# Kernel tuning notes

Measured on AMD Instinct MI355X. Metric: run time of the kernel, lower is better.

## Reference

```python
import jax, jax.numpy as jnp
import numpy as np

T, B, D = 512, 64, 1536
MAX_RADIUS = 0.999
INIT_RADIUS = 0.99
EPS = 1e-8


def setup_inputs() -> dict:
    key = jax.random.key(0)
    ks = jax.random.split(key, 5)
    # xavier_uniform bound for square [D, D] weight
    bound = float(np.sqrt(6.0 / (D + D)))
    p = INIT_RADIUS / MAX_RADIUS
    init_logit = float(np.log(p / (1.0 - p)))
    u = jax.random.normal(ks[4], (D,), dtype=jnp.float32)
    u = u / jnp.linalg.norm(u)
    return {
        "x": jax.random.normal(ks[0], (T, B, D), dtype=jnp.float32),
        "z": jax.random.normal(ks[1], (T, B, D), dtype=jnp.float32),
        "h0": jnp.zeros((B, D), dtype=jnp.float32),
        "W_x": jax.random.uniform(ks[2], (D, D), jnp.float32, -bound, bound),
        "W_h": jax.random.uniform(ks[3], (D, D), jnp.float32, -bound, bound),
        "b": jnp.zeros((D,), dtype=jnp.float32),
        "log_radius": jnp.full((1,), init_logit, dtype=jnp.float32),
        "u": u,
    }


def _spectral_norm_W_h(W_h, log_radius, u):
    """W_h scaled so its (power-iteration estimated) spectral radius = target."""
    target = jax.nn.sigmoid(log_radius)[0] * MAX_RADIUS
    # 3 power-iteration steps, done under stop_gradient (torch uses no_grad)
    v = u
    for _ in range(3):
        v = W_h.T @ u
        v = v / (jnp.linalg.norm(v) + EPS)
        u = W_h @ v
        u = u / (jnp.linalg.norm(u) + EPS)
    u = jax.lax.stop_gradient(u)
    v = jax.lax.stop_gradient(v)
    sigma = jnp.abs(u @ W_h @ v)
    return W_h * (target / (sigma + EPS))


def reference(x, z, h0, W_x, W_h, b, log_radius, u):
    Wh = _spectral_norm_W_h(W_h, log_radius, u)

    def step(h_prev, xz):
        x_t, z_t = xz  # [B, D] each
        h_new = jnp.tanh(x_t @ W_x.T + h_prev @ Wh.T + b)
        out_t = h_new * jax.nn.silu(z_t)
        return h_new, (h_new, out_t)

    _, (hs, outs) = jax.lax.scan(step, h0, (x, z))  # hs, outs: [T, B, D]
    h_all = jnp.concatenate([h0[None], hs], axis=0)  # [T+1, B, D]
    return outs, h_all
```

## Files before the change

### kernel.cpp

```cpp
#include <hip/hip_runtime.h>

#define DD 1536
#define TT 512
#define BB 64
#define BD (BB*DD)
#define TBD (TT*BD)
#define NWG 96

typedef __attribute__((ext_vector_type(8))) short short8;
typedef __attribute__((ext_vector_type(4))) float f32x4;

__device__ __forceinline__ short f2bf(float f) {
  unsigned u = __builtin_bit_cast(unsigned, f);
  u += 0x7FFFu + ((u >> 16) & 1u);
  return (short)(u >> 16);
}

__device__ __forceinline__ void st_coh_b32(int* p, int v) {
  asm volatile("global_store_dword %0, %1, off sc0 sc1" :: "v"(p), "v"(v) : "memory");
}

#define LDQ(dst, addr, imm) \
  asm volatile("global_load_dwordx4 %0, %1, off offset:" #imm " sc0 sc1" \
               : "=v"(dst) : "v"(addr) : "memory")


__global__ __launch_bounds__(256) void k_matvec_row(
    const float* __restrict__ W, const float* __restrict__ x, float* __restrict__ y) {
  int wave = (blockIdx.x * 256 + threadIdx.x) >> 6;
  int lane = threadIdx.x & 63;
  const float* Wr = W + (size_t)wave * DD;
  float acc = 0.f;
  for (int j = lane; j < DD; j += 64) acc += Wr[j] * x[j];
  for (int off = 32; off; off >>= 1) acc += __shfl_down(acc, off, 64);
  if (lane == 0) y[wave] = acc;
}

__global__ __launch_bounds__(256) void k_matvec_colf(
    const float* __restrict__ W, const float* __restrict__ x, float* __restrict__ y) {
  int j = blockIdx.x * 256 + threadIdx.x;
  float a0 = 0.f, a1 = 0.f, a2 = 0.f, a3 = 0.f;
  for (int i = 0; i < DD; i += 4) {
    a0 += W[(size_t)(i + 0) * DD + j] * x[i + 0];
    a1 += W[(size_t)(i + 1) * DD + j] * x[i + 1];
    a2 += W[(size_t)(i + 2) * DD + j] * x[i + 2];
    a3 += W[(size_t)(i + 3) * DD + j] * x[i + 3];
  }
  y[j] = (a0 + a1) + (a2 + a3);
}

__global__ __launch_bounds__(256) void k_scale(
    const float* __restrict__ t5, const float* __restrict__ t6,
    const float* __restrict__ log_radius, float* __restrict__ s_out) {
  __shared__ float red[8];
  int tid = threadIdx.x;
  float a5 = 0.f, a6 = 0.f;
  for (int i = tid; i < DD; i += 256) { float v5 = t5[i], v6 = t6[i]; a5 += v5*v5; a6 += v6*v6; }
  for (int off = 32; off; off >>= 1) { a5 += __shfl_down(a5, off, 64); a6 += __shfl_down(a6, off, 64); }
  int w = tid >> 6, lane = tid & 63;
  if (lane == 0) { red[w] = a5; red[4 + w] = a6; }
  __syncthreads();
  if (tid == 0) {
    float s5 = red[0] + red[1] + red[2] + red[3];
    float s6 = red[4] + red[5] + red[6] + red[7];
    float sigma = sqrtf(s6 / s5);
    float lr = log_radius[0];
    float target = 0.999f / (1.f + expf(-lr));
    s_out[0] = target / (sigma + 1e-8f);
  }
}

__global__ __launch_bounds__(256) void k_conv(
    const float* __restrict__ in, short* __restrict__ out, int n8) {
  int i = blockIdx.x * 256 + threadIdx.x;
  int stride = gridDim.x * 256;
  for (; i < n8; i += stride) {
    const float4* p = (const float4*)(in + (size_t)i * 8);
    float4 a = p[0], b = p[1];
    short8 v;
    v[0]=f2bf(a.x); v[1]=f2bf(a.y); v[2]=f2bf(a.z); v[3]=f2bf(a.w);
    v[4]=f2bf(b.x); v[5]=f2bf(b.y); v[6]=f2bf(b.z); v[7]=f2bf(b.w);
    *(short8*)(out + (size_t)i * 8) = v;
  }
}

__global__ __launch_bounds__(256) void k_gemm_xA(
    const float* __restrict__ x, const float* __restrict__ Wx,
    const float* __restrict__ bias, float* __restrict__ Aout) {
  __shared__ short As[128 * 64];
  __shared__ short Bs[128 * 64];
  const int tid = threadIdx.x;
  const int lane = tid & 63;
  const int w = tid >> 6;
  const int n0 = blockIdx.x * 128;
  const int m0 = blockIdx.y * 128;
  const int mq = (w >> 1) * 64;
  const int nq = (w & 1) * 64;

  f32x4 acc[4][4];
#pragma unroll
  for (int i = 0; i < 4; ++i)
#pragma unroll
    for (int j = 0; j < 4; ++j) acc[i][j] = (f32x4){0.f, 0.f, 0.f, 0.f};

  const int r0 = tid >> 3;
  const int c8 = tid & 7;

  for (int k0 = 0; k0 < DD; k0 += 64) {
    __syncthreads();
#pragma unroll
    for (int c = 0; c < 4; ++c) {
      int row = c * 32 + r0;
      const float4* gx = (const float4*)(x + (size_t)(m0 + row) * DD + k0 + c8 * 8);
      const float4* gw = (const float4*)(Wx + (size_t)(n0 + row) * DD + k0 + c8 * 8);
      float4 x0 = gx[0], x1 = gx[1];
      float4 w0 = gw[0], w1 = gw[1];
      short8 xv, wv;
      xv[0]=f2bf(x0.x); xv[1]=f2bf(x0.y); xv[2]=f2bf(x0.z); xv[3]=f2bf(x0.w);
      xv[4]=f2bf(x1.x); xv[5]=f2bf(x1.y); xv[6]=f2bf(x1.z); xv[7]=f2bf(x1.w);
      wv[0]=f2bf(w0.x); wv[1]=f2bf(w0.y); wv[2]=f2bf(w0.z); wv[3]=f2bf(w0.w);
      wv[4]=f2bf(w1.x); wv[5]=f2bf(w1.y); wv[6]=f2bf(w1.z); wv[7]=f2bf(w1.w);
      int so = (row * 64 + c8 * 8) ^ ((row & 7) << 3);
      *(short8*)&As[so] = xv;
      *(short8*)&Bs[so] = wv;
    }
    __syncthreads();
#pragma unroll
    for (int kk = 0; kk < 64; kk += 32) {
      short8 af[4], bfr[4];
#pragma unroll
      for (int f = 0; f < 4; ++f) {
        int ar = mq + f * 16 + (lane & 15);
        int k = kk + ((lane >> 4) << 3);
        af[f] = *(const short8*)&As[(ar * 64 + k) ^ ((ar & 7) << 3)];
        int br = nq + f * 16 + (lane & 15);
        bfr[f] = *(const short8*)&Bs[(br * 64 + k) ^ ((br & 7) << 3)];
      }
#pragma unroll
      for (int i = 0; i < 4; ++i)
#pragma unroll
        for (int j = 0; j < 4; ++j)
          acc[i][j] = __builtin_amdgcn_mfma_f32_16x16x32_bf16(af[i], bfr[j], acc[i][j], 0, 0, 0);
    }
  }
#pragma unroll
  for (int i = 0; i < 4; ++i) {
    int rbase = m0 + mq + i * 16 + ((lane >> 4) << 2);
#pragma unroll
    for (int j = 0; j < 4; ++j) {
      int col = n0 + nq + j * 16 + (lane & 15);
      float bv = bias[col];
#pragma unroll
      for (int r = 0; r < 4; ++r)
        Aout[(size_t)(rbase + r) * DD + col] = acc[i][j][r] + bv;
    }
  }
}

__global__ __launch_bounds__(256) void k_gemm_b(
    const short* __restrict__ xb, const short* __restrict__ Wxb,
    const float* __restrict__ bias, float* __restrict__ Aout) {
  __shared__ short As[128 * 64];
  __shared__ short Bs[128 * 64];
  const int tid = threadIdx.x;
  const int lane = tid & 63;
  const int w = tid >> 6;
  const int n0 = blockIdx.x * 128;
  const int m0 = blockIdx.y * 128;
  const int mq = (w >> 1) * 64;
  const int nq = (w & 1) * 64;

  f32x4 acc[4][4];
#pragma unroll
  for (int i = 0; i < 4; ++i)
#pragma unroll
    for (int j = 0; j < 4; ++j) acc[i][j] = (f32x4){0.f, 0.f, 0.f, 0.f};

  const int r0 = tid >> 3;
  const int c8 = tid & 7;

  for (int k0 = 0; k0 < DD; k0 += 64) {
    __syncthreads();
#pragma unroll
    for (int c = 0; c < 4; ++c) {
      int row = c * 32 + r0;
      short8 xv = *(const short8*)(xb  + (size_t)(m0 + row) * DD + k0 + c8 * 8);
      short8 wv = *(const short8*)(Wxb + (size_t)(n0 + row) * DD + k0 + c8 * 8);
      int so = (row * 64 + c8 * 8) ^ ((row & 7) << 3);
      *(short8*)&As[so] = xv;
      *(short8*)&Bs[so] = wv;
    }
    __syncthreads();
#pragma unroll
    for (int kk = 0; kk < 64; kk += 32) {
      short8 af[4], bfr[4];
#pragma unroll
      for (int f = 0; f < 4; ++f) {
        int ar = mq + f * 16 + (lane & 15);
        int k = kk + ((lane >> 4) << 3);
        af[f] = *(const short8*)&As[(ar * 64 + k) ^ ((ar & 7) << 3)];
        int br = nq + f * 16 + (lane & 15);
        bfr[f] = *(const short8*)&Bs[(br * 64 + k) ^ ((br & 7) << 3)];
      }
#pragma unroll
      for (int i = 0; i < 4; ++i)
#pragma unroll
        for (int j = 0; j < 4; ++j)
          acc[i][j] = __builtin_amdgcn_mfma_f32_16x16x32_bf16(af[i], bfr[j], acc[i][j], 0, 0, 0);
    }
  }
#pragma unroll
  for (int i = 0; i < 4; ++i) {
    int rbase = m0 + mq + i * 16 + ((lane >> 4) << 2);
#pragma unroll
    for (int j = 0; j < 4; ++j) {
      int col = n0 + nq + j * 16 + (lane & 15);
      float bv = bias[col];
#pragma unroll
      for (int r = 0; r < 4; ++r)
        Aout[(size_t)(rbase + r) * DD + col] = acc[i][j][r] + bv;
    }
  }
}

__global__ __launch_bounds__(512, 1) void k_recur(
    const float* __restrict__ Wh, const float* __restrict__ h0,
    const float* __restrict__ z, const float* __restrict__ sp,
    float* __restrict__ outs, float* __restrict__ hall,
    short* __restrict__ hbuf, int* __restrict__ flags) {
  __shared__ f32x4 REDS[2][2048];
  const int tid = threadIdx.x;
  const int lane = tid & 63;
  const int wv = tid >> 6;
  const int wgid = blockIdx.x;
  const int fg = wgid >> 2;
  const int mq = wgid & 3;
  const int n0 = fg * 64;
  const int m0 = mq * 16;

  const int nl = lane & 15;
  const int hi8 = (lane >> 4) << 3;
  const int kw = wv * 192;

  short8 bfr[6][4];
#pragma unroll
  for (int j = 0; j < 6; ++j)
#pragma unroll
    for (int f = 0; f < 4; ++f) {
      const float* gp = Wh + (size_t)(n0 + f * 16 + nl) * DD + kw + j * 32 + hi8;
      float4 a0 = *(const float4*)gp;
      float4 a1 = *(const float4*)(gp + 4);
      short8 v;
      v[0]=f2bf(a0.x); v[1]=f2bf(a0.y); v[2]=f2bf(a0.z); v[3]=f2bf(a0.w);
      v[4]=f2bf(a1.x); v[5]=f2bf(a1.y); v[6]=f2bf(a1.z); v[7]=f2bf(a1.w);
      bfr[j][f] = v;
    }

  const int r = wv + ((lane >> 5) << 3);
  const int c = (lane & 31) * 2;
  const int f0 = c >> 4;
  const int c15 = c & 15;
  const int l2a = ((r >> 2) << 4) | c15;
  const int l2b = l2a + 1;
  const int ri = r & 3;
  const size_t eidx = (size_t)(m0 + r) * DD + n0 + c;
  const size_t aoff = (size_t)(m0 + nl) * DD + kw + hi8;

  int* myflag = flags + ((mq * 24 + fg) * 8 + wv) * 16;
  const int* cflag = flags + (((mq * 24 + wv * 3 + (lane >> 3)) * 8) + (lane & 7)) * 16;

  short* pg = hbuf;
  short* pn = hbuf + BD;
  short* pq = hbuf + 2 * BD;

  {
    float vx = h0[eidx], vy = h0[eidx + 1];
    hall[eidx] = vx; hall[eidx + 1] = vy;
    unsigned pk = (unsigned)(unsigned short)f2bf(vx)
                | ((unsigned)(unsigned short)f2bf(vy) << 16);
    st_coh_b32((int*)(pg + eidx), (int)pk);
  }
  const float sv = sp[0];
  asm volatile("s_waitcnt vmcnt(0)" ::: "memory");
  if (lane == 0) st_coh_b32(myflag, 1);

  float pa = outs[eidx], pay = outs[eidx + 1];
  float pz = z[eidx], pzy = z[eidx + 1];

  for (int t = 0; t < TT; ++t) {
    const bool last = (t == TT - 1);

    if (lane < 24) {
      int it = 0;
      for (;;) {
        int v = __hip_atomic_load(cflag, __ATOMIC_RELAXED, __HIP_MEMORY_SCOPE_AGENT);
        if (v >= t + 1 || ++it > (1 << 20)) break;
        __builtin_amdgcn_s_sleep(1);
      }
    }

    const short* hp = pg + aoff;
    short8 a0, a1, a2, a3, a4, a5;
    LDQ(a0, hp, 0);
    LDQ(a1, hp, 64);
    LDQ(a2, hp, 128);
    LDQ(a3, hp, 192);
    LDQ(a4, hp, 256);
    LDQ(a5, hp, 320);
    asm volatile("s_waitcnt vmcnt(0)" ::: "memory");
    __builtin_amdgcn_sched_barrier(0);

    f32x4 acc0 = (f32x4){0,0,0,0}, acc1 = (f32x4){0,0,0,0};
    f32x4 acc2 = (f32x4){0,0,0,0}, acc3 = (f32x4){0,0,0,0};
#define MF4(aa, j) \
    acc0 = __builtin_amdgcn_mfma_f32_16x16x32_bf16(aa, bfr[j][0], acc0, 0, 0, 0); \
    acc1 = __builtin_amdgcn_mfma_f32_16x16x32_bf16(aa, bfr[j][1], acc1, 0, 0, 0); \
    acc2 = __builtin_amdgcn_mfma_f32_16x16x32_bf16(aa, bfr[j][2], acc2, 0, 0, 0); \
    acc3 = __builtin_amdgcn_mfma_f32_16x16x32_bf16(aa, bfr[j][3], acc3, 0, 0, 0);
    MF4(a0, 0) MF4(a1, 1) MF4(a2, 2) MF4(a3, 3) MF4(a4, 4) MF4(a5, 5)
#undef MF4

    f32x4* R = REDS[t & 1];
    {
      const int lsw = lane ^ ((lane >> 5) & 1);
#define WR(f, accv) { f32x4 wv_; \
      wv_[(0 + f) & 3] = accv[0]; wv_[(1 + f) & 3] = accv[1]; \
      wv_[(2 + f) & 3] = accv[2]; wv_[(3 + f) & 3] = accv[3]; \
      R[wv * 256 + f * 64 + lsw] = wv_; }
      WR(0, acc0) WR(1, acc1) WR(2, acc2) WR(3, acc3)
#undef WR
    }
    __syncthreads();
    const float* Rf = (const float*)R;
    const int ia = (f0 * 64 + (l2a ^ ((l2a >> 5) & 1))) * 4 + ((ri + f0) & 3);
    const int ib = (f0 * 64 + (l2b ^ ((l2b >> 5) & 1))) * 4 + ((ri + f0) & 3);
    float s0 = 0.f, s1 = 0.f;
#pragma unroll
    for (int w2 = 0; w2 < 8; ++w2) {
      s0 += Rf[w2 * 1024 + ia];
      s1 += Rf[w2 * 1024 + ib];
    }

    float h0v = tanhf(pa + sv * s0);
    float h1v = tanhf(pay + sv * s1);
    if (!last) {
      unsigned pk = (unsigned)(unsigned short)f2bf(h0v)
                  | ((unsigned)(unsigned short)f2bf(h1v) << 16);
      st_coh_b32((int*)(pn + eidx), (int)pk);
      asm volatile("s_waitcnt vmcnt(0)" ::: "memory");
      if (lane == 0) st_coh_b32(myflag, t + 2);
    }

    size_t tb = (size_t)t * BD;
    hall[tb + BD + eidx] = h0v;
    hall[tb + BD + eidx + 1] = h1v;
    outs[tb + eidx]     = h0v * (pz  / (1.f + __expf(-pz)));
    outs[tb + eidx + 1] = h1v * (pzy / (1.f + __expf(-pzy)));
    if (!last) {
      size_t nb = tb + BD + eidx;
      pa = outs[nb]; pay = outs[nb + 1];
      pz = z[nb];    pzy = z[nb + 1];
    }
    short* tmp = pg; pg = pn; pn = pq; pq = tmp;
  }
}

extern "C" void kernel_launch(void* const* d_in, const int* in_sizes, int n_in,
                              void* d_out, int out_size, void* d_ws, size_t ws_size,
                              hipStream_t stream) {
  const float* x  = (const float*)d_in[0];
  const float* z  = (const float*)d_in[1];
  const float* h0 = (const float*)d_in[2];
  const float* Wx = (const float*)d_in[3];
  const float* Wh = (const float*)d_in[4];
  const float* b  = (const float*)d_in[5];
  const float* lr = (const float*)d_in[6];
  const float* u  = (const float*)d_in[7];

  float* outs = (float*)d_out;
  float* hall = outs + (size_t)TBD;

  char* ws = (char*)d_ws;
  float* vA = (float*)ws;
  float* vB = vA + DD;
  float* vC = vB + DD;
  float* vD = vC + DD;
  float* sS = vD + DD;
  int*   flags = (int*)(ws + 32768);
  short* hbuf  = (short*)(ws + 131072);

  short* xb  = (short*)(ws + ((size_t)16 << 20));
  short* Wxb = xb + (size_t)TBD;
  const size_t need = ((size_t)16 << 20) + ((size_t)TBD + (size_t)DD * DD) * 2 + 1024;
  const bool big = ws_size >= need;

  if (big) {
    hipLaunchKernelGGL(k_conv, dim3(2048), dim3(256), 0, stream, x,  xb,  TBD / 8);
    hipLaunchKernelGGL(k_conv, dim3(512),  dim3(256), 0, stream, Wx, Wxb, DD * DD / 8);
    hipLaunchKernelGGL(k_gemm_b, dim3(12, 256), dim3(256), 0, stream, xb, Wxb, b, outs);
  } else {
    hipLaunchKernelGGL(k_gemm_xA, dim3(12, 256), dim3(256), 0, stream, x, Wx, b, outs);
  }

  hipLaunchKernelGGL(k_matvec_colf, dim3(6),   dim3(256), 0, stream, Wh, u,  vA);
  hipLaunchKernelGGL(k_matvec_row,  dim3(384), dim3(256), 0, stream, Wh, vA, vB);
  hipLaunchKernelGGL(k_matvec_colf, dim3(6),   dim3(256), 0, stream, Wh, vB, vA);
  hipLaunchKernelGGL(k_matvec_row,  dim3(384), dim3(256), 0, stream, Wh, vA, vB);
  hipLaunchKernelGGL(k_matvec_colf, dim3(6),   dim3(256), 0, stream, Wh, vB, vC);
  hipLaunchKernelGGL(k_matvec_row,  dim3(384), dim3(256), 0, stream, Wh, vC, vD);
  hipLaunchKernelGGL(k_scale, dim3(1), dim3(256), 0, stream, vC, vD, lr, sS);

  hipMemsetAsync(flags, 0, 49152, stream);

  void* args[8] = {(void*)&Wh, (void*)&h0, (void*)&z, (void*)&sS,
                   (void*)&outs, (void*)&hall, (void*)&hbuf, (void*)&flags};
  hipLaunchCooperativeKernel((const void*)k_recur, dim3(NWG), dim3(512), args, 0, stream);
}
```

Before: 2.466 ms.

## Fuse power-iteration matvecs and scale into one cooperative kernel

Replaces the seven small power-iteration launches (column and row matvecs plus the scale kernel) with a single 384-workgroup cooperative kernel that uses flag-based grid barriers between phases. The column matvec is split across 96 workgroups, each handling a slice of rows and combining partial sums with atomics, instead of running on only 6 blocks. The workspace is relaid out and zeroed with one memset, which replaces the separate flag memset. This targets launch overhead and the poor parallelism of the serial column matvec, at the cost of spin-wait barriers and atomic accumulation order.

```diff
diff --git a/kernel.cpp b/kernel.cpp
--- a/kernel.cpp
+++ b/kernel.cpp
@@ -24,49 +24,93 @@
   asm volatile("global_load_dwordx4 %0, %1, off offset:" #imm " sc0 sc1" \
                : "=v"(dst) : "v"(addr) : "memory")
 
-
-__global__ __launch_bounds__(256) void k_matvec_row(
-    const float* __restrict__ W, const float* __restrict__ x, float* __restrict__ y) {
-  int wave = (blockIdx.x * 256 + threadIdx.x) >> 6;
-  int lane = threadIdx.x & 63;
-  const float* Wr = W + (size_t)wave * DD;
-  float acc = 0.f;
-  for (int j = lane; j < DD; j += 64) acc += Wr[j] * x[j];
-  for (int off = 32; off; off >>= 1) acc += __shfl_down(acc, off, 64);
-  if (lane == 0) y[wave] = acc;
-}
-
-__global__ __launch_bounds__(256) void k_matvec_colf(
-    const float* __restrict__ W, const float* __restrict__ x, float* __restrict__ y) {
-  int j = blockIdx.x * 256 + threadIdx.x;
-  float a0 = 0.f, a1 = 0.f, a2 = 0.f, a3 = 0.f;
-  for (int i = 0; i < DD; i += 4) {
-    a0 += W[(size_t)(i + 0) * DD + j] * x[i + 0];
-    a1 += W[(size_t)(i + 1) * DD + j] * x[i + 1];
-    a2 += W[(size_t)(i + 2) * DD + j] * x[i + 2];
-    a3 += W[(size_t)(i + 3) * DD + j] * x[i + 3];
-  }
-  y[j] = (a0 + a1) + (a2 + a3);
-}
-
-__global__ __launch_bounds__(256) void k_scale(
-    const float* __restrict__ t5, const float* __restrict__ t6,
-    const float* __restrict__ log_radius, float* __restrict__ s_out) {
+__device__ __forceinline__ float ld_coh_f(const float* p) {
+  return __hip_atomic_load(p, __ATOMIC_RELAXED, __HIP_MEMORY_SCOPE_AGENT);
+}
+
+__global__ __launch_bounds__(256) void k_power(
+    const float* __restrict__ Wh, const float* __restrict__ u,
+    const float* __restrict__ lr, float* __restrict__ base,
+    int* __restrict__ pflags) {
   __shared__ float red[8];
-  int tid = threadIdx.x;
-  float a5 = 0.f, a6 = 0.f;
-  for (int i = tid; i < DD; i += 256) { float v5 = t5[i], v6 = t6[i]; a5 += v5*v5; a6 += v6*v6; }
-  for (int off = 32; off; off >>= 1) { a5 += __shfl_down(a5, off, 64); a6 += __shfl_down(a6, off, 64); }
-  int w = tid >> 6, lane = tid & 63;
-  if (lane == 0) { red[w] = a5; red[4 + w] = a6; }
-  __syncthreads();
-  if (tid == 0) {
-    float s5 = red[0] + red[1] + red[2] + red[3];
-    float s6 = red[4] + red[5] + red[6] + red[7];
-    float sigma = sqrtf(s6 / s5);
-    float lr = log_radius[0];
-    float target = 0.999f / (1.f + expf(-lr));
-    s_out[0] = target / (sigma + 1e-8f);
+  const int tid = threadIdx.x;
+  const int lane = tid & 63;
+  const int wgid = blockIdx.x;
+
+  float* vA = base;
+  float* vB = base + 1536;
+  float* vC = base + 3072;
+  float* vD = base + 4608;
+  float* vE = base + 6144;
+  float* vF = base + 7680;
+  float* sS = base + 9216;
+
+  auto bar = [&](int gen) {
+    asm volatile("s_waitcnt vmcnt(0)" ::: "memory");
+    __syncthreads();
+    if (tid == 0) st_coh_b32(pflags + wgid * 16, gen);
+    int it = 0;
+    for (;;) {
+      int v0 = __hip_atomic_load(pflags + tid * 16, __ATOMIC_RELAXED, __HIP_MEMORY_SCOPE_AGENT);
+      int v1 = (tid < 128)
+        ? __hip_atomic_load(pflags + (256 + tid) * 16, __ATOMIC_RELAXED, __HIP_MEMORY_SCOPE_AGENT)
+        : gen;
+      if ((v0 >= gen && v1 >= gen) || ++it > (1 << 20)) break;
+      __builtin_amdgcn_s_sleep(1);
+    }
+    __syncthreads();
+  };
+
+  auto colf = [&](const float* src, float* dst) {
+    if (wgid < 96) {
+      int jt = wgid % 6, ic = wgid / 6;
+      int j = jt * 256 + tid;
+      int i0 = ic * 96;
+      float a0 = 0.f, a1 = 0.f, a2 = 0.f, a3 = 0.f;
+      for (int i = i0; i < i0 + 96; i += 4) {
+        a0 += Wh[(size_t)(i + 0) * DD + j] * ld_coh_f(src + i + 0);
+        a1 += Wh[(size_t)(i + 1) * DD + j] * ld_coh_f(src + i + 1);
+        a2 += Wh[(size_t)(i + 2) * DD + j] * ld_coh_f(src + i + 2);
+        a3 += Wh[(size_t)(i + 3) * DD + j] * ld_coh_f(src + i + 3);
+      }
+      atomicAdd(&dst[j], (a0 + a1) + (a2 + a3));
+    }
+  };
+
+  auto rowf = [&](const float* src, float* dst) {
+    int row = wgid * 4 + (tid >> 6);
+    const float* Wr = Wh + (size_t)row * DD;
+    float acc = 0.f;
+    for (int j = lane; j < DD; j += 64) acc += Wr[j] * ld_coh_f(src + j);
+    for (int off = 32; off; off >>= 1) acc += __shfl_down(acc, off, 64);
+    if (lane == 0) st_coh_b32((int*)&dst[row], __builtin_bit_cast(int, acc));
+  };
+
+  colf(u,  vA); bar(1);
+  rowf(vA, vB); bar(2);
+  colf(vB, vC); bar(3);
+  rowf(vC, vD); bar(4);
+  colf(vD, vE); bar(5);
+  rowf(vE, vF); bar(6);
+
+  if (wgid == 0) {
+    float a5 = 0.f, a6 = 0.f;
+    for (int i = tid; i < DD; i += 256) {
+      float v5 = ld_coh_f(vE + i), v6 = ld_coh_f(vF + i);
+      a5 += v5 * v5; a6 += v6 * v6;
+    }
+    for (int off = 32; off; off >>= 1) { a5 += __shfl_down(a5, off, 64); a6 += __shfl_down(a6, off, 64); }
+    int w = tid >> 6;
+    if (lane == 0) { red[w] = a5; red[4 + w] = a6; }
+    __syncthreads();
+    if (tid == 0) {
+      float s5 = red[0] + red[1] + red[2] + red[3];
+      float s6 = red[4] + red[5] + red[6] + red[7];
+      float sigma = sqrtf(s6 / s5);
+      float lrv = lr[0];
+      float target = 0.999f / (1.f + expf(-lrv));
+      sS[0] = target / (sigma + 1e-8f);
+    }
   }
 }
 
@@ -381,18 +425,18 @@
   float* hall = outs + (size_t)TBD;
 
   char* ws = (char*)d_ws;
-  float* vA = (float*)ws;
-  float* vB = vA + DD;
-  float* vC = vB + DD;
-  float* vD = vC + DD;
-  float* sS = vD + DD;
-  int*   flags = (int*)(ws + 32768);
+  float* base  = (float*)ws;
+  float* sS    = base + 9216;
+  int*   flags = (int*)(ws + 40960);
+  int*   pflg  = (int*)(ws + 90112);
   short* hbuf  = (short*)(ws + 131072);
-
-  short* xb  = (short*)(ws + ((size_t)16 << 20));
-  short* Wxb = xb + (size_t)TBD;
-  const size_t need = ((size_t)16 << 20) + ((size_t)TBD + (size_t)DD * DD) * 2 + 1024;
+  short* xb    = (short*)(ws + ((size_t)1 << 20));
+  short* Wxb   = xb + (size_t)TBD;
+
+  const size_t need = ((size_t)1 << 20) + ((size_t)TBD + (size_t)DD * DD) * 2 + 1024;
   const bool big = ws_size >= need;
+
+  hipMemsetAsync(ws, 0, 114688, stream);
 
   if (big) {
     hipLaunchKernelGGL(k_conv, dim3(2048), dim3(256), 0, stream, x,  xb,  TBD / 8);
@@ -402,15 +446,10 @@
     hipLaunchKernelGGL(k_gemm_xA, dim3(12, 256), dim3(256), 0, stream, x, Wx, b, outs);
   }
 
-  hipLaunchKernelGGL(k_matvec_colf, dim3(6),   dim3(256), 0, stream, Wh, u,  vA);
-  hipLaunchKernelGGL(k_matvec_row,  dim3(384), dim3(256), 0, stream, Wh, vA, vB);
-  hipLaunchKernelGGL(k_matvec_colf, dim3(6),   dim3(256), 0, stream, Wh, vB, vA);
-  hipLaunchKernelGGL(k_matvec_row,  dim3(384), dim3(256), 0, stream, Wh, vA, vB);
-  hipLaunchKernelGGL(k_matvec_colf, dim3(6),   dim3(256), 0, stream, Wh, vB, vC);
-  hipLaunchKernelGGL(k_matvec_row,  dim3(384), dim3(256), 0, stream, Wh, vC, vD);
-  hipLaunchKernelGGL(k_scale, dim3(1), dim3(256), 0, stream, vC, vD, lr, sS);
-
-  hipMemsetAsync(flags, 0, 49152, stream);
+  {
+    void* pargs[5] = {(void*)&Wh, (void*)&u, (void*)&lr, (void*)&base, (void*)&pflg};
+    hipLaunchCooperativeKernel((const void*)k_power, dim3(384), dim3(256), pargs, 0, stream);
+  }
 
   void* args[8] = {(void*)&Wh, (void*)&h0, (void*)&z, (void*)&sS,
                    (void*)&outs, (void*)&hall, (void*)&hbuf, (void*)&flags};
```

After: 2.287 ms. -7.2%, faster.
